# Performance work log

Measured on AMD Instinct MI355X. Metric: run time of the kernel, lower is better.

## Reference

```python
import jax, jax.numpy as jnp
import numpy as np

NEG_INF = -1e9


def setup_inputs() -> dict:
    key = jax.random.key(0)
    k1, k2, k3 = jax.random.split(key, 3)
    B, C, Q, D = 64, 1024, 128, 128
    context = jax.random.normal(k1, (B, C, D), dtype=jnp.float32)
    query = jax.random.normal(k2, (B, Q, D), dtype=jnp.float32)
    W = jax.random.normal(k3, (3 * D, 1), dtype=jnp.float32)
    query_mask = jnp.ones((B, Q), dtype=jnp.float32)
    return {"context": context, "query": query, "W": W, "query_mask": query_mask}


def reference(context, query, W, query_mask):
    # Dense(1) over concat([c, q, c*q]) decomposes as c.w_c + q.w_q + (c*w_s).q
    D = context.shape[-1]
    w = W[:, 0]
    w_c, w_q, w_s = w[:D], w[D:2 * D], w[2 * D:]
    c_term = jnp.einsum('bcd,d->bc', context, w_c)          # [B,C]
    q_term = jnp.einsum('bqd,d->bq', query, w_q)            # [B,Q]
    s_term = jnp.einsum('bcd,bqd->bcq', context * w_s, query)  # [B,C,Q]
    S = c_term[:, :, None] + q_term[:, None, :] + s_term    # [B,C,Q]
    S = S + (1.0 - query_mask)[:, None, :] * NEG_INF
    c2q_scores = jax.nn.softmax(S, axis=2)                  # [B,C,Q]
    c2q = jnp.einsum('bcq,bqd->bcd', c2q_scores, query)     # [B,C,D]
    q2c_scores = jax.nn.softmax(jnp.max(S, axis=2), axis=1)  # [B,C]
    q2c = jnp.einsum('bc,bcd->bd', q2c_scores, context)     # [B,D]
    q2c = q2c[:, None, :]                                   # broadcast over C
    out = jnp.concatenate([context, c2q, context * c2q, context * q2c], axis=-1)
    return out
```

## Files before the change

kernel.cpp:

```cpp
#include <hip/hip_runtime.h>

#define NEGINF -1000000000.0f
#define L2E 1.44269504088896340736f

typedef __attribute__((ext_vector_type(4))) float f32x4;
typedef _Float16 half8 __attribute__((ext_vector_type(8)));
typedef _Float16 half4 __attribute__((ext_vector_type(4)));

__device__ inline float exp2fast(float x) { return __builtin_amdgcn_exp2f(x); }

constexpr int Bn = 64, Cn = 1024, Qn = 128, Dn = 128;
constexpr int QSTR = 136;
constexpr int CSTR = 132;


__global__ __launch_bounds__(512, 4) void k1_kernel(
    const float* __restrict__ ctx, const float* __restrict__ qry,
    const float* __restrict__ W, const float* __restrict__ mask,
    float* __restrict__ out, float* __restrict__ ws_part, float* __restrict__ ws_ms)
{
    __shared__ char smem[72768];
    _Float16* qrow = (_Float16*)smem;
    _Float16* qT2  = (_Float16*)(smem + 34816);
    float* wfull = (float*)(smem + 69632);
    float* qts   = (float*)(smem + 71168);
    float* mloc  = (float*)(smem + 71680);
    float* wv    = (float*)(smem + 72192);
    float* red   = (float*)(smem + 72704);
    float* cq    = (float*)smem;
    float* partf = (float*)(smem + 34816);

    const int b = blockIdx.x, cg = blockIdx.y, c0 = cg * 128;
    const int t = threadIdx.x;
    const float* ctxB = ctx + (size_t)b * Cn * Dn;
    const float* qryB = qry + (size_t)b * Qn * Dn;

    if (t < 384) wfull[t] = W[t] * L2E;
    __syncthreads();

    {
        int q = t >> 2, h = t & 3;
        const float* qr = qryB + q * Dn + h * 32;
        int p = ((q >> 5) << 5) + 8 * ((q >> 2) & 3) + (q & 3) + 4 * ((q >> 4) & 1);
        float acc = 0.f;
        for (int j = 0; j < 32; j += 4) {
            f32x4 v = *(const f32x4*)(qr + j);
            int d = h * 32 + j;
            acc += v.x * wfull[128 + d] + v.y * wfull[128 + d + 1]
                 + v.z * wfull[128 + d + 2] + v.w * wfull[128 + d + 3];
            half4 hv;
            hv[0] = (_Float16)v.x; hv[1] = (_Float16)v.y;
            hv[2] = (_Float16)v.z; hv[3] = (_Float16)v.w;
            *(half4*)&qrow[q * QSTR + d] = hv;
            qT2[(d + 0) * QSTR + p] = hv[0];
            qT2[(d + 1) * QSTR + p] = hv[1];
            qT2[(d + 2) * QSTR + p] = hv[2];
            qT2[(d + 3) * QSTR + p] = hv[3];
        }
        acc += __shfl_xor(acc, 1);
        acc += __shfl_xor(acc, 2);
        if (h == 0) qts[q] = acc + (1.0f - mask[b * Qn + q]) * (NEGINF * L2E);
    }
    __syncthreads();

    const int wave = t >> 6, lane = t & 63, g = lane >> 4, l15 = lane & 15;
    const int cw = wave * 16;
    const int cl = cw + l15;

    f32x4 acc1[8] = {};
    float cterm = 0.f;
#pragma unroll
    for (int kk = 0; kk < 4; ++kk) {
        const int dbase = kk * 32 + g * 8;
        const float* pc = ctxB + (size_t)(c0 + cl) * Dn + dbase;
        f32x4 v0 = *(const f32x4*)pc, v1 = *(const f32x4*)(pc + 4);
        f32x4 s0 = *(const f32x4*)&wfull[256 + dbase], s1 = *(const f32x4*)&wfull[256 + dbase + 4];
        f32x4 c0w = *(const f32x4*)&wfull[dbase], c1w = *(const f32x4*)&wfull[dbase + 4];
        cterm += v0.x * c0w.x + v0.y * c0w.y + v0.z * c0w.z + v0.w * c0w.w
               + v1.x * c1w.x + v1.y * c1w.y + v1.z * c1w.z + v1.w * c1w.w;
        half8 ah;
        ah[0] = (_Float16)(v0.x * s0.x); ah[1] = (_Float16)(v0.y * s0.y);
        ah[2] = (_Float16)(v0.z * s0.z); ah[3] = (_Float16)(v0.w * s0.w);
        ah[4] = (_Float16)(v1.x * s1.x); ah[5] = (_Float16)(v1.y * s1.y);
        ah[6] = (_Float16)(v1.z * s1.z); ah[7] = (_Float16)(v1.w * s1.w);
#pragma unroll
        for (int mt = 0; mt < 8; ++mt) {
            half8 qf = *(const half8*)&qrow[(mt * 16 + l15) * QSTR + dbase];
            acc1[mt] = __builtin_amdgcn_mfma_f32_16x16x32_f16(qf, ah, acc1[mt], 0, 0, 0);
        }
    }
    cterm += __shfl_xor(cterm, 16);
    cterm += __shfl_xor(cterm, 32);

#pragma unroll
    for (int mt = 0; mt < 8; ++mt)
#pragma unroll
        for (int r = 0; r < 4; ++r) acc1[mt][r] += qts[mt * 16 + g * 4 + r];

    float mx = -3.4e38f;
#pragma unroll
    for (int mt = 0; mt < 8; ++mt)
#pragma unroll
        for (int r = 0; r < 4; ++r) mx = fmaxf(mx, acc1[mt][r]);
    mx = fmaxf(mx, __shfl_xor(mx, 16));
    mx = fmaxf(mx, __shfl_xor(mx, 32));
    float sum = 0.f;
#pragma unroll
    for (int mt = 0; mt < 8; ++mt)
#pragma unroll
        for (int r = 0; r < 4; ++r) {
            float pv = exp2fast(acc1[mt][r] - mx);
            acc1[mt][r] = pv;
            sum += pv;
        }
    sum += __shfl_xor(sum, 16);
    sum += __shfl_xor(sum, 32);
    if (g == 0) mloc[cl] = mx + cterm;

    half8 pa[4];
#pragma unroll
    for (int kk2 = 0; kk2 < 4; ++kk2)
#pragma unroll
        for (int j = 0; j < 8; ++j)
            pa[kk2][j] = (_Float16)acc1[2 * kk2 + (j >> 2)][j & 3];

    float inv[4];
#pragma unroll
    for (int r = 0; r < 4; ++r) inv[r] = 1.0f / __shfl(sum, g * 4 + r);

    f32x4 acc2[8] = {};
#pragma unroll
    for (int kk2 = 0; kk2 < 4; ++kk2)
#pragma unroll
        for (int ntD = 0; ntD < 8; ++ntD) {
            half8 qb = *(const half8*)&qT2[(ntD * 16 + l15) * QSTR + kk2 * 32 + 8 * g];
            acc2[ntD] = __builtin_amdgcn_mfma_f32_16x16x32_f16(pa[kk2], qb, acc2[ntD], 0, 0, 0);
        }
    __syncthreads();

#pragma unroll
    for (int r = 0; r < 4; ++r) {
        int c = cw + g * 4 + r;
        float is = inv[r];
#pragma unroll
        for (int ntD = 0; ntD < 8; ++ntD)
            cq[c * CSTR + ntD * 16 + l15] = acc2[ntD][r] * is;
    }
    __syncthreads();

    const int grp = t >> 5, d4 = (t & 31) * 4;
#pragma unroll
    for (int step = 0; step < 8; ++step) {
        int c = grp + step * 16;
        f32x4 q = *(const f32x4*)&cq[c * CSTR + d4];
        f32x4 cv = *(const f32x4*)(ctxB + (size_t)(c0 + c) * Dn + d4);
        float* orow = out + ((size_t)(b * Cn + c0 + c)) * 512;
        *(f32x4*)(orow + d4) = cv;
        *(f32x4*)(orow + 128 + d4) = q;
        f32x4 pr;
        pr.x = cv.x * q.x; pr.y = cv.y * q.y; pr.z = cv.z * q.z; pr.w = cv.w * q.w;
        *(f32x4*)(orow + 256 + d4) = pr;
    }

    float vm = mloc[t & 127];
    float m = vm;
#pragma unroll
    for (int off = 1; off < 64; off <<= 1) m = fmaxf(m, __shfl_xor(m, off));
    if (lane == 0) red[wave] = m;
    __syncthreads();
    float Mloc = red[0];
#pragma unroll
    for (int i = 1; i < 8; ++i) Mloc = fmaxf(Mloc, red[i]);
    float e = exp2fast(vm - Mloc);
    if (t < 128) wv[t] = e;
    float s = e;
#pragma unroll
    for (int off = 1; off < 64; off <<= 1) s += __shfl_xor(s, off);
    if (lane == 0) red[8 + wave] = s;
    __syncthreads();
    float Sloc = red[8] + red[9];

    {
        const float* cb = ctxB + (size_t)(c0 + grp * 8) * Dn;
        f32x4 a = {};
#pragma unroll
        for (int i = 0; i < 8; ++i) {
            f32x4 cv = *(const f32x4*)(cb + (size_t)i * Dn + d4);
            float w = wv[grp * 8 + i];
            a.x += w * cv.x; a.y += w * cv.y; a.z += w * cv.z; a.w += w * cv.w;
        }
        *(f32x4*)&partf[grp * 128 + d4] = a;
    }
    __syncthreads();
    if (t < 128) {
        float s2 = 0.f;
#pragma unroll
        for (int g2 = 0; g2 < 16; ++g2) s2 += partf[g2 * 128 + t];
        ws_part[((size_t)(b * 8 + cg)) * 128 + t] = s2;
    }
    if (t == 0) {
        ws_ms[(b * 8 + cg) * 2 + 0] = Mloc;
        ws_ms[(b * 8 + cg) * 2 + 1] = Sloc;
    }
}

__global__ __launch_bounds__(256) void k3_kernel(
    const float* __restrict__ ctx, const float* __restrict__ ws_part,
    const float* __restrict__ ws_ms, float* __restrict__ out)
{
    __shared__ float q2cs[128];
    const int ct = blockIdx.x, b = blockIdx.y, t = threadIdx.x;
    if (t < 128) {
        const float* ms = ws_ms + b * 16;
        float Mg = -3.4e38f;
#pragma unroll
        for (int i = 0; i < 8; ++i) Mg = fmaxf(Mg, ms[2 * i]);
        float num = 0.f, den = 0.f;
#pragma unroll
        for (int i = 0; i < 8; ++i) {
            float e = exp2fast(ms[2 * i] - Mg);
            num += e * ws_part[((size_t)(b * 8 + i)) * 128 + t];
            den += e * ms[2 * i + 1];
        }
        q2cs[t] = num / den;
    }
    __syncthreads();
    const float* cb = ctx + ((size_t)b * Cn + ct * 128) * Dn;
    float* ob = out + ((size_t)(b * Cn) + ct * 128) * 512;
    for (int step = 0; step < 16; ++step) {
        int c = (t >> 5) + step * 8, d4 = (t & 31) * 4;
        f32x4 v = *(const f32x4*)(cb + (size_t)c * Dn + d4);
        f32x4 q = *(const f32x4*)&q2cs[d4];
        f32x4 w;
        w.x = v.x * q.x; w.y = v.y * q.y; w.z = v.z * q.z; w.w = v.w * q.w;
        *(f32x4*)(ob + (size_t)c * 512 + 384 + d4) = w;
    }
}

extern "C" void kernel_launch(void* const* d_in, const int* in_sizes, int n_in,
                              void* d_out, int out_size, void* d_ws, size_t ws_size,
                              hipStream_t stream) {
    const float* ctx  = (const float*)d_in[0];
    const float* qry  = (const float*)d_in[1];
    const float* W    = (const float*)d_in[2];
    const float* mask = (const float*)d_in[3];
    float* out = (float*)d_out;

    float* ws_part = (float*)d_ws;
    float* ws_ms   = ws_part + (size_t)Bn * 8 * 128;

    k1_kernel<<<dim3(Bn, 8), 512, 0, stream>>>(ctx, qry, W, mask, out, ws_part, ws_ms);
    k3_kernel<<<dim3(8, Bn), 256, 0, stream>>>(ctx, ws_part, ws_ms, out);
}
```

Baseline: 48.70 us.

## Fuse q2c epilogue into main kernel via per-batch atomic counter barrier

Drops the separate k3 kernel. The 8 column-group blocks of each batch now sync through a global atomic counter and spin-wait, then each block computes the q2c softmax combine and writes its own context*q2c slice. A tiny reset kernel zeroes the counters before each launch. This removes one launch and re-reads context rows the block already touched, but it relies on all 8 blocks of a batch being resident at once to avoid deadlock, and blocks idle while they spin.

```diff
diff --git a/kernel.cpp b/kernel.cpp
--- a/kernel.cpp
+++ b/kernel.cpp
@@ -13,13 +13,18 @@
 constexpr int QSTR = 136;
 constexpr int CSTR = 132;
 
+__global__ void reset_kernel(unsigned* __restrict__ cnt) {
+    cnt[threadIdx.x] = 0u;
+}
+
 
 __global__ __launch_bounds__(512, 4) void k1_kernel(
     const float* __restrict__ ctx, const float* __restrict__ qry,
     const float* __restrict__ W, const float* __restrict__ mask,
-    float* __restrict__ out, float* __restrict__ ws_part, float* __restrict__ ws_ms)
+    float* __restrict__ out, float* __restrict__ ws_part,
+    float* __restrict__ ws_ms, unsigned* __restrict__ cnt)
 {
-    __shared__ char smem[72768];
+    __shared__ char smem[73280];
     _Float16* qrow = (_Float16*)smem;
     _Float16* qT2  = (_Float16*)(smem + 34816);
     float* wfull = (float*)(smem + 69632);
@@ -27,6 +32,7 @@
     float* mloc  = (float*)(smem + 71680);
     float* wv    = (float*)(smem + 72192);
     float* red   = (float*)(smem + 72704);
+    float* q2cs  = (float*)(smem + 72768);
     float* cq    = (float*)smem;
     float* partf = (float*)(smem + 34816);
 
@@ -196,44 +202,54 @@
         float s2 = 0.f;
 #pragma unroll
         for (int g2 = 0; g2 < 16; ++g2) s2 += partf[g2 * 128 + t];
-        ws_part[((size_t)(b * 8 + cg)) * 128 + t] = s2;
+        __hip_atomic_store(&ws_part[((size_t)(b * 8 + cg)) * 128 + t], s2,
+                           __ATOMIC_RELAXED, __HIP_MEMORY_SCOPE_AGENT);
     }
     if (t == 0) {
-        ws_ms[(b * 8 + cg) * 2 + 0] = Mloc;
-        ws_ms[(b * 8 + cg) * 2 + 1] = Sloc;
-    }
-}
-
-__global__ __launch_bounds__(256) void k3_kernel(
-    const float* __restrict__ ctx, const float* __restrict__ ws_part,
-    const float* __restrict__ ws_ms, float* __restrict__ out)
-{
-    __shared__ float q2cs[128];
-    const int ct = blockIdx.x, b = blockIdx.y, t = threadIdx.x;
+        __hip_atomic_store(&ws_ms[(b * 8 + cg) * 2 + 0], Mloc,
+                           __ATOMIC_RELAXED, __HIP_MEMORY_SCOPE_AGENT);
+        __hip_atomic_store(&ws_ms[(b * 8 + cg) * 2 + 1], Sloc,
+                           __ATOMIC_RELAXED, __HIP_MEMORY_SCOPE_AGENT);
+    }
+    __syncthreads();
+
+    if (t == 0) {
+        __threadfence();
+        __hip_atomic_fetch_add(&cnt[b], 1u, __ATOMIC_ACQ_REL, __HIP_MEMORY_SCOPE_AGENT);
+        while (__hip_atomic_load(&cnt[b], __ATOMIC_ACQUIRE, __HIP_MEMORY_SCOPE_AGENT) < 8u)
+            __builtin_amdgcn_s_sleep(1);
+    }
+    __syncthreads();
+
     if (t < 128) {
-        const float* ms = ws_ms + b * 16;
+        float msv[16];
+#pragma unroll
+        for (int i = 0; i < 16; ++i)
+            msv[i] = __hip_atomic_load(&ws_ms[b * 16 + i],
+                                       __ATOMIC_RELAXED, __HIP_MEMORY_SCOPE_AGENT);
         float Mg = -3.4e38f;
 #pragma unroll
-        for (int i = 0; i < 8; ++i) Mg = fmaxf(Mg, ms[2 * i]);
+        for (int i = 0; i < 8; ++i) Mg = fmaxf(Mg, msv[2 * i]);
         float num = 0.f, den = 0.f;
 #pragma unroll
         for (int i = 0; i < 8; ++i) {
-            float e = exp2fast(ms[2 * i] - Mg);
-            num += e * ws_part[((size_t)(b * 8 + i)) * 128 + t];
-            den += e * ms[2 * i + 1];
+            float e2 = exp2fast(msv[2 * i] - Mg);
+            num += e2 * __hip_atomic_load(&ws_part[((size_t)(b * 8 + i)) * 128 + t],
+                                          __ATOMIC_RELAXED, __HIP_MEMORY_SCOPE_AGENT);
+            den += e2 * msv[2 * i + 1];
         }
         q2cs[t] = num / den;
     }
     __syncthreads();
-    const float* cb = ctx + ((size_t)b * Cn + ct * 128) * Dn;
-    float* ob = out + ((size_t)(b * Cn) + ct * 128) * 512;
-    for (int step = 0; step < 16; ++step) {
-        int c = (t >> 5) + step * 8, d4 = (t & 31) * 4;
-        f32x4 v = *(const f32x4*)(cb + (size_t)c * Dn + d4);
-        f32x4 q = *(const f32x4*)&q2cs[d4];
+
+#pragma unroll
+    for (int step = 0; step < 8; ++step) {
+        int c = grp + step * 16;
+        f32x4 cv = *(const f32x4*)(ctxB + (size_t)(c0 + c) * Dn + d4);
+        f32x4 qv = *(const f32x4*)&q2cs[d4];
         f32x4 w;
-        w.x = v.x * q.x; w.y = v.y * q.y; w.z = v.z * q.z; w.w = v.w * q.w;
-        *(f32x4*)(ob + (size_t)c * 512 + 384 + d4) = w;
+        w.x = cv.x * qv.x; w.y = cv.y * qv.y; w.z = cv.z * qv.z; w.w = cv.w * qv.w;
+        *(f32x4*)(out + ((size_t)(b * Cn + c0 + c)) * 512 + 384 + d4) = w;
     }
 }
 
@@ -248,7 +264,8 @@
 
     float* ws_part = (float*)d_ws;
     float* ws_ms   = ws_part + (size_t)Bn * 8 * 128;
-
-    k1_kernel<<<dim3(Bn, 8), 512, 0, stream>>>(ctx, qry, W, mask, out, ws_part, ws_ms);
-    k3_kernel<<<dim3(8, Bn), 256, 0, stream>>>(ctx, ws_part, ws_ms, out);
+    unsigned* cnt  = (unsigned*)(ws_ms + (size_t)Bn * 16);
+
+    reset_kernel<<<dim3(1), 64, 0, stream>>>(cnt);
+    k1_kernel<<<dim3(Bn, 8), 512, 0, stream>>>(ctx, qry, W, mask, out, ws_part, ws_ms, cnt);
 }
```

New measurement: 105.8 us. 117% more time.
